# Optimization experiments

Hardware: AMD Instinct MI355X
Metric: run time of the kernel (lower is better)

## Reference

```python
import jax, jax.numpy as jnp
import numpy as np

ADAPT_RATE = 0.1
RECOVERY_RATE = 0.1


def setup_inputs() -> dict:
    key = jax.random.key(0)
    B, T, F = 32, 512, 4096
    x = jax.random.normal(key, (B, T, F), dtype=jnp.float32)
    adaptation = jnp.zeros((1, F), dtype=jnp.float32)
    return {"x": x, "adaptation": adaptation}


def reference(x, adaptation):
    # x: [B, T, F]; adaptation param: [1, F] broadcast to [B, F]
    B, T, F = x.shape
    adapt0 = jnp.broadcast_to(adaptation, (B, F))

    def step(adapt, frame):
        out = jnp.maximum(frame - adapt, 0.0)          # clamp(min=0)
        adapt = (adapt + ADAPT_RATE * out) * (1.0 - RECOVERY_RATE)
        return adapt, out

    xs = jnp.swapaxes(x, 0, 1)                          # [T, B, F]
    _, outs = jax.lax.scan(step, adapt0, xs)            # outs: [T, B, F]
    return jnp.swapaxes(outs, 0, 1)                     # [B, T, F]
```

## Files before the change

### kernel.cpp

```cpp
#include <hip/hip_runtime.h>


#define AB 32
#define AT 512
#define AF 4096
#define ADAPT_RATE 0.1f
#define RECOVERY_RATE 0.1f

__global__ __launch_bounds__(256) void AdaptiveLayer_kernel(
    const float* __restrict__ x,
    const float* __restrict__ adaptation,
    float* __restrict__ out) {
    const int tid = blockIdx.x * blockDim.x + threadIdx.x;
    const int b = tid >> 12;
    const int f = tid & (AF - 1);

    float adapt = adaptation[f];

    const size_t base = (size_t)b * (size_t)AT * (size_t)AF + (size_t)f;
    const float* __restrict__ xp = x + base;
    float* __restrict__ op = out + base;

    #pragma unroll 1
    for (int t = 0; t < AT; t += 8) {
        float v[8];
        #pragma unroll
        for (int j = 0; j < 8; ++j) {
            v[j] = xp[(size_t)(t + j) * AF];
        }
        #pragma unroll
        for (int j = 0; j < 8; ++j) {
            float o = fmaxf(v[j] - adapt, 0.0f);
            op[(size_t)(t + j) * AF] = o;
            adapt = (adapt + ADAPT_RATE * o) * (1.0f - RECOVERY_RATE);
        }
    }
}

extern "C" void kernel_launch(void* const* d_in, const int* in_sizes, int n_in,
                              void* d_out, int out_size, void* d_ws, size_t ws_size,
                              hipStream_t stream) {
    const float* x          = (const float*)d_in[0];
    const float* adaptation = (const float*)d_in[1];
    float* out              = (float*)d_out;

    const int n_chains = AB * AF;
    const int block = 256;
    const int grid = n_chains / block;

    AdaptiveLayer_kernel<<<grid, block, 0, stream>>>(x, adaptation, out);
}
```

Before: 444.2 us.

## Vectorize chains to float4 with double-buffered nontemporal loads and stores

Each thread now processes four adjacent feature chains using 128-bit loads and stores, and prefetches the next 8 timesteps while computing the current 8. Loads and stores use nontemporal hints to avoid cache pollution. This raises the bytes in flight per thread to hide memory latency on a serial recurrence. The cost is 4x fewer threads and blocks (block size 128), which lowers occupancy and wave-level parallelism across CUs.

```diff
diff --git a/kernel.cpp b/kernel.cpp
--- a/kernel.cpp
+++ b/kernel.cpp
@@ -4,35 +4,72 @@
 #define AB 32
 #define AT 512
 #define AF 4096
+#define F4 (AF / 4)
 #define ADAPT_RATE 0.1f
 #define RECOVERY_RATE 0.1f
 
-__global__ __launch_bounds__(256) void AdaptiveLayer_kernel(
+typedef float f32x4 __attribute__((ext_vector_type(4)));
+
+__global__ __launch_bounds__(128) void AdaptiveLayer_kernel(
     const float* __restrict__ x,
     const float* __restrict__ adaptation,
     float* __restrict__ out) {
     const int tid = blockIdx.x * blockDim.x + threadIdx.x;
-    const int b = tid >> 12;
-    const int f = tid & (AF - 1);
+    const int b  = tid >> 10;
+    const int f4 = tid & (F4 - 1);
 
-    float adapt = adaptation[f];
+    const size_t base4 = (size_t)b * (size_t)AT * (size_t)F4 + (size_t)f4;
+    const f32x4* __restrict__ xp = reinterpret_cast<const f32x4*>(x) + base4;
+    f32x4* __restrict__ op       = reinterpret_cast<f32x4*>(out) + base4;
 
-    const size_t base = (size_t)b * (size_t)AT * (size_t)AF + (size_t)f;
-    const float* __restrict__ xp = x + base;
-    float* __restrict__ op = out + base;
+    f32x4 adapt = reinterpret_cast<const f32x4*>(adaptation)[f4];
+
+    f32x4 bufA[8], bufB[8];
+
+    #pragma unroll
+    for (int j = 0; j < 8; ++j)
+        bufA[j] = __builtin_nontemporal_load(xp + (size_t)j * F4);
 
     #pragma unroll 1
-    for (int t = 0; t < AT; t += 8) {
-        float v[8];
+    for (int t = 0; t < AT; t += 16) {
+        #pragma unroll
+        for (int j = 0; j < 8; ++j)
+            bufB[j] = __builtin_nontemporal_load(xp + (size_t)(t + 8 + j) * F4);
+
         #pragma unroll
         for (int j = 0; j < 8; ++j) {
-            v[j] = xp[(size_t)(t + j) * AF];
+            f32x4 v = bufA[j];
+            f32x4 o;
+            o.x = fmaxf(v.x - adapt.x, 0.0f);
+            o.y = fmaxf(v.y - adapt.y, 0.0f);
+            o.z = fmaxf(v.z - adapt.z, 0.0f);
+            o.w = fmaxf(v.w - adapt.w, 0.0f);
+            __builtin_nontemporal_store(o, op + (size_t)(t + j) * F4);
+            adapt.x = (adapt.x + ADAPT_RATE * o.x) * (1.0f - RECOVERY_RATE);
+            adapt.y = (adapt.y + ADAPT_RATE * o.y) * (1.0f - RECOVERY_RATE);
+            adapt.z = (adapt.z + ADAPT_RATE * o.z) * (1.0f - RECOVERY_RATE);
+            adapt.w = (adapt.w + ADAPT_RATE * o.w) * (1.0f - RECOVERY_RATE);
         }
+
+        if (t + 16 < AT) {
+            #pragma unroll
+            for (int j = 0; j < 8; ++j)
+                bufA[j] = __builtin_nontemporal_load(xp + (size_t)(t + 16 + j) * F4);
+        }
+
         #pragma unroll
         for (int j = 0; j < 8; ++j) {
-            float o = fmaxf(v[j] - adapt, 0.0f);
-            op[(size_t)(t + j) * AF] = o;
-            adapt = (adapt + ADAPT_RATE * o) * (1.0f - RECOVERY_RATE);
+            f32x4 v = bufB[j];
+            f32x4 o;
+            o.x = fmaxf(v.x - adapt.x, 0.0f);
+            o.y = fmaxf(v.y - adapt.y, 0.0f);
+            o.z = fmaxf(v.z - adapt.z, 0.0f);
+            o.w = fmaxf(v.w - adapt.w, 0.0f);
+            __builtin_nontemporal_store(o, op + (size_t)(t + 8 + j) * F4);
+            adapt.x = (adapt.x + ADAPT_RATE * o.x) * (1.0f - RECOVERY_RATE);
+            adapt.y = (adapt.y + ADAPT_RATE * o.y) * (1.0f - RECOVERY_RATE);
+            adapt.z = (adapt.z + ADAPT_RATE * o.z) * (1.0f - RECOVERY_RATE);
+            adapt.w = (adapt.w + ADAPT_RATE * o.w) * (1.0f - RECOVERY_RATE);
         }
     }
 }
@@ -44,8 +81,8 @@
     const float* adaptation = (const float*)d_in[1];
     float* out              = (float*)d_out;
 
-    const int n_chains = AB * AF;
-    const int block = 256;
+    const int n_chains = AB * F4;
+    const int block = 128;
     const int grid = n_chains / block;
 
     AdaptiveLayer_kernel<<<grid, block, 0, stream>>>(x, adaptation, out);
```

Result: faster. 422.6 us (-4.9%).
